# Kernel tuning notes

Measured on AMD Instinct MI355X. Metric: run time of the kernel, lower is better.

## Reference

```python
import jax, jax.numpy as jnp
import numpy as np

B, L, D, UNITS = 512, 64, 1024, 512

def setup_inputs() -> dict:
    key = jax.random.key(0)
    ks = jax.random.split(key, 8)
    sc = lambda n: 1.0 / np.sqrt(n)
    return {
        "features": jax.random.normal(ks[0], (B, L, D), jnp.float32),
        "hidden": jax.random.normal(ks[1], (B, UNITS), jnp.float32),
        "W1_w": jax.random.normal(ks[2], (D, UNITS), jnp.float32) * sc(D),
        "W1_b": jnp.zeros((UNITS,), jnp.float32),
        "W2_w": jax.random.normal(ks[3], (UNITS, UNITS), jnp.float32) * sc(UNITS),
        "W2_b": jnp.zeros((UNITS,), jnp.float32),
        "V_w": jax.random.normal(ks[4], (UNITS, 1), jnp.float32) * sc(UNITS),
        "V_b": jnp.zeros((1,), jnp.float32),
    }

def reference(features, hidden, W1_w, W1_b, W2_w, W2_b, V_w, V_b):
    # features: [B, L, D], hidden: [B, U]
    h = hidden @ W2_w + W2_b                      # [B, U]
    score = jnp.tanh(features @ W1_w + W1_b + h[:, None, :])  # [B, L, U]
    logits = score @ V_w + V_b                    # [B, L, 1]
    attn = jax.nn.softmax(logits, axis=1)         # softmax over L
    context = jnp.sum(attn * features, axis=1)    # [B, D]
    return context, attn
```

## Files before the change

### kernel.cpp

```cpp
#include <hip/hip_runtime.h>
#include <hip/hip_bf16.h>

#define Bb 512
#define Ll 64
#define Dd 1024
#define Uu 512

typedef __attribute__((ext_vector_type(8))) short short8;
typedef __attribute__((ext_vector_type(4))) float f32x4;
typedef __attribute__((ext_vector_type(4))) unsigned short u16x4;

__device__ __forceinline__ unsigned short f2bf(float x) {
  unsigned int u = __float_as_uint(x);
  u += 0x7FFF + ((u >> 16) & 1);
  return (unsigned short)(u >> 16);
}

__global__ void k_hidden(const float* __restrict__ hidden,
                         const float* __restrict__ W2w,
                         const float* __restrict__ W2b,
                         float* __restrict__ h) {
  __shared__ float hid[8][Uu];
  const int b0 = blockIdx.x * 8;
  const int u = threadIdx.x;
  for (int i = 0; i < 8; ++i) hid[i][u] = hidden[(size_t)(b0 + i) * Uu + u];
  __syncthreads();
  float acc[8] = {0.f, 0.f, 0.f, 0.f, 0.f, 0.f, 0.f, 0.f};
  for (int k = 0; k < Uu; ++k) {
    const float w = W2w[(size_t)k * Uu + u];
#pragma unroll 8
    for (int i = 0; i < 8; ++i) acc[i] += hid[i][k] * w;
  }
  const float bb = W2b[u];
  for (int i = 0; i < 8; ++i) h[(size_t)(b0 + i) * Uu + u] = acc[i] + bb;
}

__global__ void k_w1t(const float* __restrict__ W1w, unsigned short* __restrict__ W1T) {
  __shared__ float tile[32][33];
  const int kb = blockIdx.x;
  const int ub = blockIdx.y;
  const int t = threadIdx.x;
#pragma unroll
  for (int i = 0; i < 4; ++i) {
    const int idx = t + i * 256;
    const int r = idx >> 5, c = idx & 31;
    tile[r][c] = W1w[(size_t)(kb * 32 + r) * Uu + ub * 32 + c];
  }
  __syncthreads();
#pragma unroll
  for (int i = 0; i < 4; ++i) {
    const int idx = t + i * 256;
    const int ur = idx >> 5, kc = idx & 31;
    W1T[(size_t)(ub * 32 + ur) * Dd + kb * 32 + kc] = f2bf(tile[kc][ur]);
  }
}

__global__ void __launch_bounds__(512) k_fused(
    const float* __restrict__ features,
    const unsigned short* __restrict__ W1T,
    const float* __restrict__ W1b,
    const float* __restrict__ h,
    const float* __restrict__ Vw,
    const float* __restrict__ Vb,
    float* __restrict__ out_ctx,
    float* __restrict__ out_attn) {
  __shared__ __align__(16) unsigned char smem[73728];
  unsigned char* smA = smem;
  unsigned char* smB = smem + 8192;
  float (*lp)[8] = (float(*)[8])smem;
  float* attn_s = (float*)(smem + 2048);

  const int b = blockIdx.x;
  const int tid = threadIdx.x;
  const int lane = tid & 63;
  const int w = tid >> 6;
  const int l15 = lane & 15;
  const int lg = lane >> 4;

  const float* featB = features + (size_t)b * Ll * Dd;

  f32x4 acc[4][4];
#pragma unroll
  for (int mi = 0; mi < 4; ++mi)
#pragma unroll
    for (int ni = 0; ni < 4; ++ni) acc[mi][ni] = (f32x4){0.f, 0.f, 0.f, 0.f};

  for (int kt = 0; kt < Dd / 64; ++kt) {
    const int k0 = kt * 64;
#pragma unroll
    for (int i = 0; i < 2; ++i) {
      const int c = tid + i * 512;
      const int row = c >> 4;
      const int pos = c & 15;
      const float4 v = *reinterpret_cast<const float4*>(featB + (size_t)row * Dd + k0 + pos * 4);
      u16x4 p = {f2bf(v.x), f2bf(v.y), f2bf(v.z), f2bf(v.w)};
      const int slot = pos >> 1;
      *reinterpret_cast<u16x4*>(smA + row * 128 + ((slot ^ (row & 7)) << 4) + (pos & 1) * 8) = p;
    }
#pragma unroll
    for (int i = 0; i < 8; ++i) {
      const int c = i * 512 + tid;
      const int uu = c >> 3;
      const int ch = c & 7;
      const int4 v = *reinterpret_cast<const int4*>(W1T + (size_t)uu * Dd + k0 + ch * 8);
      *reinterpret_cast<int4*>(smB + uu * 128 + ((ch ^ (uu & 7)) << 4)) = v;
    }
    __syncthreads();
#pragma unroll
    for (int kk = 0; kk < 2; ++kk) {
      const int slot = kk * 4 + lg;
      short8 afr[4], bfr[4];
#pragma unroll
      for (int mi = 0; mi < 4; ++mi) {
        const int row = mi * 16 + l15;
        afr[mi] = *reinterpret_cast<const short8*>(smA + row * 128 + ((slot ^ (row & 7)) << 4));
      }
#pragma unroll
      for (int ni = 0; ni < 4; ++ni) {
        const int uu = w * 64 + ni * 16 + l15;
        bfr[ni] = *reinterpret_cast<const short8*>(smB + uu * 128 + ((slot ^ (uu & 7)) << 4));
      }
#pragma unroll
      for (int mi = 0; mi < 4; ++mi)
#pragma unroll
        for (int ni = 0; ni < 4; ++ni)
          acc[mi][ni] = __builtin_amdgcn_mfma_f32_16x16x32_bf16(afr[mi], bfr[ni], acc[mi][ni], 0, 0, 0);
    }
    __syncthreads();
  }

  float part[4][4];
#pragma unroll
  for (int mi = 0; mi < 4; ++mi)
#pragma unroll
    for (int r = 0; r < 4; ++r) part[mi][r] = 0.f;

#pragma unroll
  for (int ni = 0; ni < 4; ++ni) {
    const int col = w * 64 + ni * 16 + l15;
    const float hb = h[(size_t)b * Uu + col];
    const float b1 = W1b[col];
    const float vw = Vw[col];
#pragma unroll
    for (int mi = 0; mi < 4; ++mi) {
#pragma unroll
      for (int r = 0; r < 4; ++r) {
        const float x = acc[mi][ni][r] + b1 + hb;
        const float e = __expf(2.f * x);
        part[mi][r] += vw * (e - 1.f) / (e + 1.f);
      }
    }
  }
#pragma unroll
  for (int mi = 0; mi < 4; ++mi)
#pragma unroll
    for (int r = 0; r < 4; ++r) {
      float v = part[mi][r];
      v += __shfl_xor(v, 1);
      v += __shfl_xor(v, 2);
      v += __shfl_xor(v, 4);
      v += __shfl_xor(v, 8);
      if (l15 == 0) lp[mi * 16 + lg * 4 + r][w] = v;
    }
  __syncthreads();

  if (tid < 64) {
    float lgv = Vb[0];
#pragma unroll
    for (int j = 0; j < 8; ++j) lgv += lp[tid][j];
    float m = lgv;
#pragma unroll
    for (int off = 32; off > 0; off >>= 1) m = fmaxf(m, __shfl_xor(m, off));
    const float e = __expf(lgv - m);
    float s = e;
#pragma unroll
    for (int off = 32; off > 0; off >>= 1) s += __shfl_xor(s, off);
    const float a = e / s;
    attn_s[tid] = a;
    out_attn[(size_t)b * 64 + tid] = a;
  }
  __syncthreads();

  const int d0 = tid * 2;
  float2 c2 = {0.f, 0.f};
#pragma unroll 8
  for (int l = 0; l < 64; ++l) {
    const float a = attn_s[l];
    const float2 f = *reinterpret_cast<const float2*>(featB + (size_t)l * Dd + d0);
    c2.x += a * f.x;
    c2.y += a * f.y;
  }
  *reinterpret_cast<float2*>(out_ctx + (size_t)b * Dd + d0) = c2;
}

extern "C" void kernel_launch(void* const* d_in, const int* in_sizes, int n_in,
                              void* d_out, int out_size, void* d_ws, size_t ws_size,
                              hipStream_t stream) {
  const float* features = (const float*)d_in[0];
  const float* hidden   = (const float*)d_in[1];
  const float* W1w      = (const float*)d_in[2];
  const float* W1b      = (const float*)d_in[3];
  const float* W2w      = (const float*)d_in[4];
  const float* W2b      = (const float*)d_in[5];
  const float* Vw       = (const float*)d_in[6];
  const float* Vb       = (const float*)d_in[7];
  float* out_ctx  = (float*)d_out;
  float* out_attn = (float*)d_out + (size_t)Bb * Dd;

  float* h = (float*)d_ws;
  unsigned short* W1T = (unsigned short*)((char*)d_ws + (size_t)Bb * Uu * 4);

  k_hidden<<<64, 512, 0, stream>>>(hidden, W2w, W2b, h);
  k_w1t<<<dim3(32, 16), 256, 0, stream>>>(W1w, W1T);
  k_fused<<<Bb, 512, 0, stream>>>(features, W1T, W1b, h, Vw, Vb, out_ctx, out_attn);
}
```

Measured before the change: 321.7 us.

## Merge prep kernels, double-buffer GEMM with direct-to-LDS loads, two batches per block

Merges the hidden projection and the W1 transpose into one prep kernel. W1 is stored in per-k-tile swizzled bf16 chunks so the fused kernel can copy it straight into LDS with global_load_lds. The fused kernel now runs 1024 threads on two batch rows per block, double-buffers A and B tiles across 32-wide k steps with register prefetch of features, and shares each W1 tile between both batches. The tanh formula is simplified to one division. The aim is to cut W1 reload traffic per batch, overlap loads with MFMA work, and drop one launch, at the cost of fewer blocks (256) and more LDS per block.

```diff
diff --git a/kernel.cpp b/kernel.cpp
--- a/kernel.cpp
+++ b/kernel.cpp
@@ -16,68 +16,109 @@
   return (unsigned short)(u >> 16);
 }
 
-__global__ void k_hidden(const float* __restrict__ hidden,
-                         const float* __restrict__ W2w,
-                         const float* __restrict__ W2b,
-                         float* __restrict__ h) {
-  __shared__ float hid[8][Uu];
-  const int b0 = blockIdx.x * 8;
-  const int u = threadIdx.x;
-  for (int i = 0; i < 8; ++i) hid[i][u] = hidden[(size_t)(b0 + i) * Uu + u];
-  __syncthreads();
-  float acc[8] = {0.f, 0.f, 0.f, 0.f, 0.f, 0.f, 0.f, 0.f};
-  for (int k = 0; k < Uu; ++k) {
-    const float w = W2w[(size_t)k * Uu + u];
-#pragma unroll 8
-    for (int i = 0; i < 8; ++i) acc[i] += hid[i][k] * w;
-  }
-  const float bb = W2b[u];
-  for (int i = 0; i < 8; ++i) h[(size_t)(b0 + i) * Uu + u] = acc[i] + bb;
-}
-
-__global__ void k_w1t(const float* __restrict__ W1w, unsigned short* __restrict__ W1T) {
-  __shared__ float tile[32][33];
-  const int kb = blockIdx.x;
-  const int ub = blockIdx.y;
+__device__ __forceinline__ void gld16(const void* g, void* l) {
+  auto gp = reinterpret_cast<const __attribute__((address_space(1))) unsigned int*>(
+      reinterpret_cast<uintptr_t>(g));
+  auto lp = reinterpret_cast<__attribute__((address_space(3))) unsigned int*>(
+      reinterpret_cast<uintptr_t>(l));
+  __builtin_amdgcn_global_load_lds(gp, lp, 16, 0, 0);
+}
+
+__global__ void __launch_bounds__(512) k_prep(const float* __restrict__ hidden,
+                                              const float* __restrict__ W2w,
+                                              const float* __restrict__ W2b,
+                                              const float* __restrict__ W1w,
+                                              float* __restrict__ h,
+                                              unsigned char* __restrict__ W1s) {
   const int t = threadIdx.x;
-#pragma unroll
-  for (int i = 0; i < 4; ++i) {
-    const int idx = t + i * 256;
-    const int r = idx >> 5, c = idx & 31;
-    tile[r][c] = W1w[(size_t)(kb * 32 + r) * Uu + ub * 32 + c];
-  }
-  __syncthreads();
-#pragma unroll
-  for (int i = 0; i < 4; ++i) {
-    const int idx = t + i * 256;
-    const int ur = idx >> 5, kc = idx & 31;
-    W1T[(size_t)(ub * 32 + ur) * Dd + kb * 32 + kc] = f2bf(tile[kc][ur]);
-  }
-}
-
-__global__ void __launch_bounds__(512) k_fused(
+  if (blockIdx.x < 128) {
+    __shared__ float hid[4][Uu];
+    const int b0 = blockIdx.x * 4;
+#pragma unroll
+    for (int i = 0; i < 4; ++i) hid[i][t] = hidden[(size_t)(b0 + i) * Uu + t];
+    __syncthreads();
+    float a0 = 0.f, a1 = 0.f, a2 = 0.f, a3 = 0.f;
+    for (int k0 = 0; k0 < Uu; k0 += 8) {
+      float wv[8];
+#pragma unroll
+      for (int j = 0; j < 8; ++j) wv[j] = W2w[(size_t)(k0 + j) * Uu + t];
+#pragma unroll
+      for (int j = 0; j < 8; ++j) {
+        a0 += hid[0][k0 + j] * wv[j];
+        a1 += hid[1][k0 + j] * wv[j];
+        a2 += hid[2][k0 + j] * wv[j];
+        a3 += hid[3][k0 + j] * wv[j];
+      }
+    }
+    const float bb = W2b[t];
+    h[(size_t)(b0 + 0) * Uu + t] = a0 + bb;
+    h[(size_t)(b0 + 1) * Uu + t] = a1 + bb;
+    h[(size_t)(b0 + 2) * Uu + t] = a2 + bb;
+    h[(size_t)(b0 + 3) * Uu + t] = a3 + bb;
+  } else {
+    const int id = blockIdx.x - 128;
+    const int kb = id >> 3;
+    const int ub = id & 7;
+    __shared__ float tile[32][68];
+    {
+      const int r = t >> 4;
+      const int c4 = t & 15;
+      const float4 v = *reinterpret_cast<const float4*>(
+          &W1w[(size_t)(kb * 32 + r) * Uu + ub * 64 + c4 * 4]);
+      *reinterpret_cast<float4*>(&tile[r][c4 * 4]) = v;
+    }
+    __syncthreads();
+    if (t < 256) {
+      const int ul = t >> 2;
+      const int ch = t & 3;
+      const int u = ub * 64 + ul;
+      unsigned int px[4];
+#pragma unroll
+      for (int q = 0; q < 4; ++q) {
+        const unsigned int lo = f2bf(tile[ch * 8 + q * 2][ul]);
+        const unsigned int hi = f2bf(tile[ch * 8 + q * 2 + 1][ul]);
+        px[q] = lo | (hi << 16);
+      }
+      const int sw = ch ^ (u & 3);
+      uint4 pack;
+      pack.x = px[0]; pack.y = px[1]; pack.z = px[2]; pack.w = px[3];
+      *reinterpret_cast<uint4*>(&W1s[(size_t)kb * 32768 + u * 64 + sw * 16]) = pack;
+    }
+  }
+}
+
+__global__ void __launch_bounds__(1024) k_fused(
     const float* __restrict__ features,
-    const unsigned short* __restrict__ W1T,
+    const unsigned char* __restrict__ W1s,
     const float* __restrict__ W1b,
     const float* __restrict__ h,
     const float* __restrict__ Vw,
     const float* __restrict__ Vb,
     float* __restrict__ out_ctx,
     float* __restrict__ out_attn) {
-  __shared__ __align__(16) unsigned char smem[73728];
-  unsigned char* smA = smem;
-  unsigned char* smB = smem + 8192;
-  float (*lp)[8] = (float(*)[8])smem;
-  float* attn_s = (float*)(smem + 2048);
-
-  const int b = blockIdx.x;
+  __shared__ __align__(16) unsigned char smem[81920];
+  unsigned char* bufA = smem;
+  unsigned char* bufB = smem + 16384;
+
+  const int b0 = blockIdx.x * 2;
   const int tid = threadIdx.x;
   const int lane = tid & 63;
   const int w = tid >> 6;
+  const int wr = w >> 3;
+  const int wc = w & 7;
   const int l15 = lane & 15;
   const int lg = lane >> 4;
 
-  const float* featB = features + (size_t)b * Ll * Dd;
+  const float* featB = features + (size_t)b0 * Ll * Dd;
+
+  const int ar = tid >> 3;
+  const int ap = tid & 7;
+  const float* ag = featB + (size_t)ar * Dd + ap * 4;
+  const int awoff = ar * 64 + (((ap >> 1) ^ (ar & 3)) << 4) + (ap & 1) * 8;
+
+  const int swl = (lg ^ (l15 & 3)) << 4;
+  const int aoff0 = (wr * 64 + l15) * 64 + swl;
+  const int boff0 = (wc * 64 + l15) * 64 + swl;
 
   f32x4 acc[4][4];
 #pragma unroll
@@ -85,48 +126,46 @@
 #pragma unroll
     for (int ni = 0; ni < 4; ++ni) acc[mi][ni] = (f32x4){0.f, 0.f, 0.f, 0.f};
 
-  for (int kt = 0; kt < Dd / 64; ++kt) {
-    const int k0 = kt * 64;
-#pragma unroll
-    for (int i = 0; i < 2; ++i) {
-      const int c = tid + i * 512;
-      const int row = c >> 4;
-      const int pos = c & 15;
-      const float4 v = *reinterpret_cast<const float4*>(featB + (size_t)row * Dd + k0 + pos * 4);
-      u16x4 p = {f2bf(v.x), f2bf(v.y), f2bf(v.z), f2bf(v.w)};
-      const int slot = pos >> 1;
-      *reinterpret_cast<u16x4*>(smA + row * 128 + ((slot ^ (row & 7)) << 4) + (pos & 1) * 8) = p;
-    }
-#pragma unroll
-    for (int i = 0; i < 8; ++i) {
-      const int c = i * 512 + tid;
-      const int uu = c >> 3;
-      const int ch = c & 7;
-      const int4 v = *reinterpret_cast<const int4*>(W1T + (size_t)uu * Dd + k0 + ch * 8);
-      *reinterpret_cast<int4*>(smB + uu * 128 + ((ch ^ (uu & 7)) << 4)) = v;
+  {
+    const float4 va = *reinterpret_cast<const float4*>(ag);
+    const unsigned char* src = W1s + (size_t)(w * 2) * 1024 + lane * 16;
+    unsigned char* dst = bufB + (w * 2) * 1024;
+    gld16(src, dst);
+    gld16(src + 1024, dst + 1024);
+    u16x4 pa = {f2bf(va.x), f2bf(va.y), f2bf(va.z), f2bf(va.w)};
+    *reinterpret_cast<u16x4*>(bufA + awoff) = pa;
+  }
+  __syncthreads();
+
+  for (int kt = 0; kt < 32; ++kt) {
+    const int cur = kt & 1;
+    const unsigned char* cA = bufA + cur * 8192;
+    const unsigned char* cB = bufB + cur * 32768;
+    float4 va;
+    if (kt < 31) {
+      va = *reinterpret_cast<const float4*>(ag + (kt + 1) * 32);
+      const unsigned char* src = W1s + (size_t)(kt + 1) * 32768 + (w * 2) * 1024 + lane * 16;
+      unsigned char* dst = bufB + (cur ^ 1) * 32768 + (w * 2) * 1024;
+      gld16(src, dst);
+      gld16(src + 1024, dst + 1024);
+    }
+    short8 afr[4], bfr[4];
+#pragma unroll
+    for (int mi = 0; mi < 4; ++mi)
+      afr[mi] = *reinterpret_cast<const short8*>(cA + aoff0 + mi * 1024);
+#pragma unroll
+    for (int ni = 0; ni < 4; ++ni)
+      bfr[ni] = *reinterpret_cast<const short8*>(cB + boff0 + ni * 1024);
+#pragma unroll
+    for (int mi = 0; mi < 4; ++mi)
+#pragma unroll
+      for (int ni = 0; ni < 4; ++ni)
+        acc[mi][ni] = __builtin_amdgcn_mfma_f32_16x16x32_bf16(afr[mi], bfr[ni], acc[mi][ni], 0, 0, 0);
+    if (kt < 31) {
+      u16x4 pa = {f2bf(va.x), f2bf(va.y), f2bf(va.z), f2bf(va.w)};
+      *reinterpret_cast<u16x4*>(bufA + (cur ^ 1) * 8192 + awoff) = pa;
     }
     __syncthreads();
-#pragma unroll
-    for (int kk = 0; kk < 2; ++kk) {
-      const int slot = kk * 4 + lg;
-      short8 afr[4], bfr[4];
-#pragma unroll
-      for (int mi = 0; mi < 4; ++mi) {
-        const int row = mi * 16 + l15;
-        afr[mi] = *reinterpret_cast<const short8*>(smA + row * 128 + ((slot ^ (row & 7)) << 4));
-      }
-#pragma unroll
-      for (int ni = 0; ni < 4; ++ni) {
-        const int uu = w * 64 + ni * 16 + l15;
-        bfr[ni] = *reinterpret_cast<const short8*>(smB + uu * 128 + ((slot ^ (uu & 7)) << 4));
-      }
-#pragma unroll
-      for (int mi = 0; mi < 4; ++mi)
-#pragma unroll
-        for (int ni = 0; ni < 4; ++ni)
-          acc[mi][ni] = __builtin_amdgcn_mfma_f32_16x16x32_bf16(afr[mi], bfr[ni], acc[mi][ni], 0, 0, 0);
-    }
-    __syncthreads();
   }
 
   float part[4][4];
@@ -135,22 +174,24 @@
 #pragma unroll
     for (int r = 0; r < 4; ++r) part[mi][r] = 0.f;
 
+  const int bt = b0 + wr;
 #pragma unroll
   for (int ni = 0; ni < 4; ++ni) {
-    const int col = w * 64 + ni * 16 + l15;
-    const float hb = h[(size_t)b * Uu + col];
+    const int col = wc * 64 + ni * 16 + l15;
+    const float hb = h[(size_t)bt * Uu + col];
     const float b1 = W1b[col];
     const float vw = Vw[col];
 #pragma unroll
-    for (int mi = 0; mi < 4; ++mi) {
+    for (int mi = 0; mi < 4; ++mi)
 #pragma unroll
       for (int r = 0; r < 4; ++r) {
         const float x = acc[mi][ni][r] + b1 + hb;
         const float e = __expf(2.f * x);
-        part[mi][r] += vw * (e - 1.f) / (e + 1.f);
+        part[mi][r] += vw * (1.f - 2.f / (e + 1.f));
       }
-    }
-  }
+  }
+  float* lpart = (float*)smem;
+  float* attn_s = (float*)(smem + 4096);
 #pragma unroll
   for (int mi = 0; mi < 4; ++mi)
 #pragma unroll
@@ -160,14 +201,16 @@
       v += __shfl_xor(v, 2);
       v += __shfl_xor(v, 4);
       v += __shfl_xor(v, 8);
-      if (l15 == 0) lp[mi * 16 + lg * 4 + r][w] = v;
+      if (l15 == 0) lpart[(wr * 64 + mi * 16 + lg * 4 + r) * 8 + wc] = v;
     }
   __syncthreads();
 
-  if (tid < 64) {
+  if (tid < 128) {
+    const int bi = tid >> 6;
+    const int row = tid & 63;
     float lgv = Vb[0];
 #pragma unroll
-    for (int j = 0; j < 8; ++j) lgv += lp[tid][j];
+    for (int j = 0; j < 8; ++j) lgv += lpart[(bi * 64 + row) * 8 + j];
     float m = lgv;
 #pragma unroll
     for (int off = 32; off > 0; off >>= 1) m = fmaxf(m, __shfl_xor(m, off));
@@ -177,20 +220,24 @@
     for (int off = 32; off > 0; off >>= 1) s += __shfl_xor(s, off);
     const float a = e / s;
     attn_s[tid] = a;
-    out_attn[(size_t)b * 64 + tid] = a;
+    out_attn[(size_t)(b0 + bi) * 64 + row] = a;
   }
   __syncthreads();
 
-  const int d0 = tid * 2;
-  float2 c2 = {0.f, 0.f};
+  {
+    const int bi = tid >> 9;
+    const int dq = tid & 511;
+    const float* fb = features + (size_t)(b0 + bi) * Ll * Dd + dq * 2;
+    float2 c2 = {0.f, 0.f};
 #pragma unroll 8
-  for (int l = 0; l < 64; ++l) {
-    const float a = attn_s[l];
-    const float2 f = *reinterpret_cast<const float2*>(featB + (size_t)l * Dd + d0);
-    c2.x += a * f.x;
-    c2.y += a * f.y;
-  }
-  *reinterpret_cast<float2*>(out_ctx + (size_t)b * Dd + d0) = c2;
+    for (int l = 0; l < 64; ++l) {
+      const float a = attn_s[bi * 64 + l];
+      const float2 f = *reinterpret_cast<const float2*>(fb + (size_t)l * Dd);
+      c2.x += a * f.x;
+      c2.y += a * f.y;
+    }
+    *reinterpret_cast<float2*>(&out_ctx[(size_t)(b0 + bi) * Dd + dq * 2]) = c2;
+  }
 }
 
 extern "C" void kernel_launch(void* const* d_in, const int* in_sizes, int n_in,
@@ -208,9 +255,8 @@
   float* out_attn = (float*)d_out + (size_t)Bb * Dd;
 
   float* h = (float*)d_ws;
-  unsigned short* W1T = (unsigned short*)((char*)d_ws + (size_t)Bb * Uu * 4);
-
-  k_hidden<<<64, 512, 0, stream>>>(hidden, W2w, W2b, h);
-  k_w1t<<<dim3(32, 16), 256, 0, stream>>>(W1w, W1T);
-  k_fused<<<Bb, 512, 0, stream>>>(features, W1T, W1b, h, Vw, Vb, out_ctx, out_attn);
-}
+  unsigned char* W1s = (unsigned char*)d_ws + (1u << 20);
+
+  k_prep<<<384, 512, 0, stream>>>(hidden, W2w, W2b, W1w, h, W1s);
+  k_fused<<<256, 1024, 0, stream>>>(features, W1s, W1b, h, Vw, Vb, out_ctx, out_attn);
+}
```

Result: faster. 285.5 us (-11.2%).
